# Kernel tuning notes

Measured on AMD Instinct MI355X. Metric: run time of the kernel, lower is better.

Reference implementation:

```python
import jax, jax.numpy as jnp
import numpy as np

K = 7  # SMorph filter size


def _smorph(x, w, alpha):
    # x: [B,1,H,W]; w: [K,K]; alpha: scalar
    # SMorph(x)(p) = sum_s (x(p+s)+w(s)) * exp(alpha*(x(p+s)+w(s))) / sum_s exp(...)
    patches = jax.lax.conv_general_dilated_patches(
        x, filter_shape=(K, K), window_strides=(1, 1), padding='SAME')  # [B,K*K,H,W]
    z = patches + w.reshape(1, K * K, 1, 1)
    wts = jax.nn.softmax(alpha * z, axis=1)
    out = jnp.sum(z * wts, axis=1, keepdims=True)  # [B,1,H,W]
    return out


def _pool2(x):
    # 2x2 average pool, stride 2; x: [...,H,W]
    B, C, H, W = x.shape
    return x.reshape(B, C, H // 2, 2, W // 2, 2).mean(axis=(3, 5))


def setup_inputs() -> dict:
    key = jax.random.key(0)
    ks = jax.random.split(key, 9)
    B = 512
    return {
        'x': jax.random.normal(ks[0], (B, 1, 28, 28), dtype=jnp.float32),
        'sm_w': 0.5 * jax.random.normal(ks[1], (8, 2, K, K), dtype=jnp.float32),
        'sm_alpha': jax.random.uniform(ks[2], (8, 2), dtype=jnp.float32),
        'W1': jax.random.normal(ks[3], (120, 392), dtype=jnp.float32) / np.sqrt(392),
        'b1': jax.random.normal(ks[4], (120,), dtype=jnp.float32) * 0.01,
        'W2': jax.random.normal(ks[5], (84, 120), dtype=jnp.float32) / np.sqrt(120),
        'b2': jax.random.normal(ks[6], (84,), dtype=jnp.float32) * 0.01,
        'W3': jax.random.normal(ks[7], (10, 84), dtype=jnp.float32) / np.sqrt(84),
        'b3': jax.random.normal(ks[8], (10,), dtype=jnp.float32) * 0.01,
    }


def reference(x, sm_w, sm_alpha, W1, b1, W2, b2, W3, b3):
    B = x.shape[0]

    def branch(w2, a2):
        y = _smorph(x, w2[0], a2[0])
        y = _smorph(y, w2[1], a2[1])
        y = _pool2(_pool2(y))  # [B,1,7,7]
        return y

    ys = jax.vmap(branch)(sm_w, sm_alpha)  # [8,B,1,7,7]
    feat = jnp.transpose(ys, (1, 0, 2, 3, 4)).reshape(B, -1)  # [B,392] = concat(x1..x8)
    h = jax.nn.sigmoid(feat @ W1.T + b1)
    h = jax.nn.sigmoid(h @ W2.T + b2)
    out = jax.nn.sigmoid(h @ W3.T + b3)
    return out
```

## Files before the change

### kernel.cpp

```cpp
#include <hip/hip_runtime.h>

#define HW 28
#define NPIX 784
#define NB 512
#define PADW2 34
#define PADH 34
#define IMG_U (PADH * PADW2)

__device__ __forceinline__ void conv2col(const unsigned* sbuf,
                                         unsigned wpack,
                                         int R0, int c, float o0[7], float o1[7])
{
    const uint2* rq0 = (const uint2*)(sbuf + R0 * PADW2 + 2 * c);
    uint2 p0 = rq0[0], p1 = rq0[1], p2 = rq0[2], p3 = rq0[3];

    unsigned Wq[49];
#pragma unroll
    for (int i = 0; i < 49; ++i)
        Wq[i] = __builtin_amdgcn_readlane(wpack, i);

    float num0[7], num1[7], den0[7], den1[7];
#pragma unroll
    for (int r = 0; r < 7; ++r) {
        num0[r] = 0.f; num1[r] = 0.f; den0[r] = 0.f; den1[r] = 0.f;
    }

#pragma unroll
    for (int rr = 0; rr < 13; ++rr) {
        uint2 n0, n1, n2, n3;
        if (rr < 12) {
            const uint2* rq = (const uint2*)(sbuf + (R0 + rr + 1) * PADW2 + 2 * c);
            n0 = rq[0]; n1 = rq[1]; n2 = rq[2]; n3 = rq[3];
            __builtin_amdgcn_sched_barrier(0);
        }
        unsigned tp[8] = {p0.x, p0.y, p1.x, p1.y, p2.x, p2.y, p3.x, p3.y};
#pragma unroll
        for (int r = 0; r < 7; ++r) {
            if (r > rr || rr - r > 6) continue;
            const int di = rr - r;
#pragma unroll
            for (int t = 0; t < 7; ++t) {
                unsigned wq = Wq[di * 7 + t];
                unsigned wd;
                asm("s_lshr_b32 %0, %1, 16" : "=s"(wd) : "s"(wq));
                asm("v_dot2_f32_f16 %0, %1, %2, %0"
                    : "+v"(num0[r]) : "v"(tp[t]),     "s"(wq));
                asm("v_dot2_f32_f16 %0, %1, %2, %0"
                    : "+v"(num1[r]) : "v"(tp[t + 1]), "s"(wq));
                asm("v_dot2_f32_f16 %0, %1, %2, %0"
                    : "+v"(den0[r]) : "v"(tp[t]),     "s"(wd));
                asm("v_dot2_f32_f16 %0, %1, %2, %0"
                    : "+v"(den1[r]) : "v"(tp[t + 1]), "s"(wd));
            }
        }
        if (rr < 12) { p0 = n0; p1 = n1; p2 = n2; p3 = n3; }
    }
#pragma unroll
    for (int r = 0; r < 7; ++r) {
        o0[r] = num0[r] * __builtin_amdgcn_rcpf(den0[r]);
        o1[r] = num1[r] * __builtin_amdgcn_rcpf(den1[r]);
    }
}

__device__ __forceinline__ float sigmoidf_(float s) {
    return __builtin_amdgcn_rcpf(1.f + __expf(-s));
}

__global__ __launch_bounds__(512, 2) void smorph_net_kernel(
    const float* __restrict__ x,
    const float* __restrict__ sw,
    const float* __restrict__ sa,
    const float* __restrict__ W1, const float* __restrict__ b1,
    const float* __restrict__ W2, const float* __restrict__ b2,
    const float* __restrict__ W3, const float* __restrict__ b3,
    float* __restrict__ out)
{
    __shared__ __align__(16) unsigned bufs[8][IMG_U];
    __shared__ __align__(16) float    mlp[392 + 120 + 128];

    const int b    = blockIdx.x;
    const int tid  = threadIdx.x;
    const int f    = tid >> 6;
    const int lane = tid & 63;

    unsigned* buf = bufs[f];
    const float* src = x + (size_t)b * NPIX;

    const float a1 = sa[f * 2 + 0];
    const float a2 = sa[f * 2 + 1];

    unsigned wp1 = 0, wp2 = 0;
    if (lane < 49) {
        union { _Float16 h[2]; unsigned u; } p;
        float w1v = sw[(f * 2 + 0) * 49 + lane];
        float e1  = __expf(a1 * w1v);
        p.h[0] = (_Float16)(w1v * e1);
        p.h[1] = (_Float16)e1;
        wp1 = p.u;
        float w2v = sw[(f * 2 + 1) * 49 + lane];
        float e2  = __expf(a2 * w2v);
        p.h[0] = (_Float16)(w2v * e2);
        p.h[1] = (_Float16)e2;
        wp2 = p.u;
    }

    for (int idx = lane; idx < IMG_U; idx += 64)
        buf[idx] = 0x00003C00u;

#pragma unroll
    for (int k = 0; k < 13; ++k) {
        int p = lane + 64 * k;
        if (p < NPIX) {
            float v = src[p];
            int pi = p / HW;
            int pj = p - pi * HW;
            float e = __expf(a1 * v);
            union { _Float16 h[2]; unsigned u; } pk;
            pk.h[0] = (_Float16)e;
            pk.h[1] = (_Float16)(v * e);
            buf[(pi + 3) * PADW2 + (pj + 3)] = pk.u;
        }
    }

    const bool act = (lane < 56);
    const int s  = lane / 14;
    const int c  = lane - s * 14;
    const int R0 = 7 * s;
    const int j2 = 2 * c;

    float o0[7], o1[7];
    if (act) conv2col(buf, wp1, R0, c, o0, o1);

    if (act) {
#pragma unroll
        for (int r = 0; r < 7; ++r) {
            union { _Float16 h[2]; unsigned u; } pk;
            float e0 = __expf(a2 * o0[r]);
            pk.h[0] = (_Float16)e0; pk.h[1] = (_Float16)(o0[r] * e0);
            buf[(R0 + r + 3) * PADW2 + (j2 + 3)] = pk.u;
            float e1 = __expf(a2 * o1[r]);
            pk.h[0] = (_Float16)e1; pk.h[1] = (_Float16)(o1[r] * e1);
            buf[(R0 + r + 3) * PADW2 + (j2 + 4)] = pk.u;
        }
    }

    if (act) conv2col(buf, wp2, R0, c, o0, o1);

    float* outp = (float*)buf;
    if (act) {
#pragma unroll
        for (int r = 0; r < 7; ++r) {
            outp[(R0 + r) * HW + j2]     = o0[r];
            outp[(R0 + r) * HW + j2 + 1] = o1[r];
        }
    }

    float* feat = mlp;
    float* h1   = mlp + 392;
    float* h2   = mlp + 512;

    if (lane < 49) {
        int pi = lane / 7;
        int pj = lane - pi * 7;
        float poolsum = 0.f;
#pragma unroll
        for (int di = 0; di < 4; ++di)
#pragma unroll
            for (int dj = 0; dj < 4; ++dj)
                poolsum += outp[(pi * 4 + di) * HW + (pj * 4 + dj)];
        feat[f * 49 + lane] = poolsum * 0.0625f;
    }
    __syncthreads();

    if (tid < 480) {
        int n = tid >> 2, h = tid & 3;
        const float4* wr = (const float4*)(W1 + n * 392);
        const float4* fv = (const float4*)feat;
        float c0 = 0.f, c1 = 0.f, c2 = 0.f, c3 = 0.f;
        for (int k = h; k < 98; k += 4) {
            float4 w = wr[k];
            float4 v = fv[k];
            c0 = fmaf(w.x, v.x, c0);
            c1 = fmaf(w.y, v.y, c1);
            c2 = fmaf(w.z, v.z, c2);
            c3 = fmaf(w.w, v.w, c3);
        }
        float acc = (c0 + c1) + (c2 + c3);
        acc += __shfl_xor(acc, 1);
        acc += __shfl_xor(acc, 2);
        if (h == 0) h1[n] = sigmoidf_(acc + b1[n]);
    }
    __syncthreads();

    if (tid < 336) {
        int n = tid >> 2, h = tid & 3;
        const float4* wr = (const float4*)(W2 + n * 120);
        const float4* hv = (const float4*)h1;
        float c0 = 0.f, c1 = 0.f, c2 = 0.f, c3 = 0.f;
        for (int k = h; k < 30; k += 4) {
            float4 w = wr[k];
            float4 v = hv[k];
            c0 = fmaf(w.x, v.x, c0);
            c1 = fmaf(w.y, v.y, c1);
            c2 = fmaf(w.z, v.z, c2);
            c3 = fmaf(w.w, v.w, c3);
        }
        float acc = (c0 + c1) + (c2 + c3);
        acc += __shfl_xor(acc, 1);
        acc += __shfl_xor(acc, 2);
        if (h == 0) h2[n] = sigmoidf_(acc + b2[n]);
    }
    __syncthreads();

    if (tid < 40) {
        int n = tid >> 2, q = tid & 3;
        const float4* wr = (const float4*)(W3 + n * 84);
        const float4* hv = (const float4*)h2;
        float c0 = 0.f, c1 = 0.f, c2 = 0.f, c3 = 0.f;
        for (int k = q; k < 21; k += 4) {
            float4 w = wr[k];
            float4 v = hv[k];
            c0 = fmaf(w.x, v.x, c0);
            c1 = fmaf(w.y, v.y, c1);
            c2 = fmaf(w.z, v.z, c2);
            c3 = fmaf(w.w, v.w, c3);
        }
        float acc = (c0 + c1) + (c2 + c3);
        acc += __shfl_xor(acc, 1);
        acc += __shfl_xor(acc, 2);
        if (q == 0) out[(size_t)b * 10 + n] = sigmoidf_(acc + b3[n]);
    }
}

extern "C" void kernel_launch(void* const* d_in, const int* in_sizes, int n_in,
                              void* d_out, int out_size, void* d_ws, size_t ws_size,
                              hipStream_t stream) {
    const float* x  = (const float*)d_in[0];
    const float* sw = (const float*)d_in[1];
    const float* sa = (const float*)d_in[2];
    const float* W1 = (const float*)d_in[3];
    const float* b1 = (const float*)d_in[4];
    const float* W2 = (const float*)d_in[5];
    const float* b2 = (const float*)d_in[6];
    const float* W3 = (const float*)d_in[7];
    const float* b3 = (const float*)d_in[8];
    float* out = (float*)d_out;

    smorph_net_kernel<<<NB, 512, 0, stream>>>(x, sw, sa, W1, b1, W2, b2, W3, b3, out);
}
```

Baseline: 101.1 us.

## Split each filter branch across two wavefronts, one output column each

```diff
diff --git a/kernel.cpp b/kernel.cpp
--- a/kernel.cpp
+++ b/kernel.cpp
@@ -7,9 +7,10 @@
 #define PADH 34
 #define IMG_U (PADH * PADW2)
 
-__device__ __forceinline__ void conv2col(const unsigned* sbuf,
+template<int P>
+__device__ __forceinline__ void conv1col(const unsigned* sbuf,
                                          unsigned wpack,
-                                         int R0, int c, float o0[7], float o1[7])
+                                         int R0, int c, float o[7])
 {
     const uint2* rq0 = (const uint2*)(sbuf + R0 * PADW2 + 2 * c);
     uint2 p0 = rq0[0], p1 = rq0[1], p2 = rq0[2], p3 = rq0[3];
@@ -19,11 +20,9 @@
     for (int i = 0; i < 49; ++i)
         Wq[i] = __builtin_amdgcn_readlane(wpack, i);
 
-    float num0[7], num1[7], den0[7], den1[7];
-#pragma unroll
-    for (int r = 0; r < 7; ++r) {
-        num0[r] = 0.f; num1[r] = 0.f; den0[r] = 0.f; den1[r] = 0.f;
-    }
+    float num[7], den[7];
+#pragma unroll
+    for (int r = 0; r < 7; ++r) { num[r] = 0.f; den[r] = 0.f; }
 
 #pragma unroll
     for (int rr = 0; rr < 13; ++rr) {
@@ -44,29 +43,23 @@
                 unsigned wd;
                 asm("s_lshr_b32 %0, %1, 16" : "=s"(wd) : "s"(wq));
                 asm("v_dot2_f32_f16 %0, %1, %2, %0"
-                    : "+v"(num0[r]) : "v"(tp[t]),     "s"(wq));
+                    : "+v"(num[r]) : "v"(tp[t + P]), "s"(wq));
                 asm("v_dot2_f32_f16 %0, %1, %2, %0"
-                    : "+v"(num1[r]) : "v"(tp[t + 1]), "s"(wq));
-                asm("v_dot2_f32_f16 %0, %1, %2, %0"
-                    : "+v"(den0[r]) : "v"(tp[t]),     "s"(wd));
-                asm("v_dot2_f32_f16 %0, %1, %2, %0"
-                    : "+v"(den1[r]) : "v"(tp[t + 1]), "s"(wd));
+                    : "+v"(den[r]) : "v"(tp[t + P]), "s"(wd));
             }
         }
         if (rr < 12) { p0 = n0; p1 = n1; p2 = n2; p3 = n3; }
     }
 #pragma unroll
-    for (int r = 0; r < 7; ++r) {
-        o0[r] = num0[r] * __builtin_amdgcn_rcpf(den0[r]);
-        o1[r] = num1[r] * __builtin_amdgcn_rcpf(den1[r]);
-    }
+    for (int r = 0; r < 7; ++r)
+        o[r] = num[r] * __builtin_amdgcn_rcpf(den[r]);
 }
 
 __device__ __forceinline__ float sigmoidf_(float s) {
     return __builtin_amdgcn_rcpf(1.f + __expf(-s));
 }
 
-__global__ __launch_bounds__(512, 2) void smorph_net_kernel(
+__global__ __launch_bounds__(1024, 2) void smorph_net_kernel(
     const float* __restrict__ x,
     const float* __restrict__ sw,
     const float* __restrict__ sa,
@@ -80,8 +73,10 @@
 
     const int b    = blockIdx.x;
     const int tid  = threadIdx.x;
-    const int f    = tid >> 6;
+    const int f    = tid >> 7;
+    const int t128 = tid & 127;
     const int lane = tid & 63;
+    const int P    = (t128 >> 6);
 
     unsigned* buf = bufs[f];
     const float* src = x + (size_t)b * NPIX;
@@ -104,12 +99,20 @@
         wp2 = p.u;
     }
 
-    for (int idx = lane; idx < IMG_U; idx += 64)
-        buf[idx] = 0x00003C00u;
-
-#pragma unroll
-    for (int k = 0; k < 13; ++k) {
-        int p = lane + 64 * k;
+    {
+        uint4* b4 = (uint4*)buf;
+        const uint4 fv = make_uint4(0x00003C00u, 0x00003C00u, 0x00003C00u, 0x00003C00u);
+#pragma unroll
+        for (int k = 0; k < 3; ++k) {
+            int i = t128 + 128 * k;
+            if (i < IMG_U / 4) b4[i] = fv;
+        }
+    }
+    __syncthreads();
+
+#pragma unroll
+    for (int k = 0; k < 7; ++k) {
+        int p = t128 + 128 * k;
         if (p < NPIX) {
             float v = src[p];
             int pi = p / HW;
@@ -121,45 +124,51 @@
             buf[(pi + 3) * PADW2 + (pj + 3)] = pk.u;
         }
     }
+    __syncthreads();
 
     const bool act = (lane < 56);
     const int s  = lane / 14;
     const int c  = lane - s * 14;
     const int R0 = 7 * s;
-    const int j2 = 2 * c;
-
-    float o0[7], o1[7];
-    if (act) conv2col(buf, wp1, R0, c, o0, o1);
+    const int j  = 2 * c + P;
+
+    float o[7];
+    if (act) {
+        if (P == 0) conv1col<0>(buf, wp1, R0, c, o);
+        else        conv1col<1>(buf, wp1, R0, c, o);
+    }
+    __syncthreads();
 
     if (act) {
 #pragma unroll
         for (int r = 0; r < 7; ++r) {
             union { _Float16 h[2]; unsigned u; } pk;
-            float e0 = __expf(a2 * o0[r]);
-            pk.h[0] = (_Float16)e0; pk.h[1] = (_Float16)(o0[r] * e0);
-            buf[(R0 + r + 3) * PADW2 + (j2 + 3)] = pk.u;
-            float e1 = __expf(a2 * o1[r]);
-            pk.h[0] = (_Float16)e1; pk.h[1] = (_Float16)(o1[r] * e1);
-            buf[(R0 + r + 3) * PADW2 + (j2 + 4)] = pk.u;
-        }
-    }
-
-    if (act) conv2col(buf, wp2, R0, c, o0, o1);
+            float e0 = __expf(a2 * o[r]);
+            pk.h[0] = (_Float16)e0; pk.h[1] = (_Float16)(o[r] * e0);
+            buf[(R0 + r + 3) * PADW2 + (j + 3)] = pk.u;
+        }
+    }
+    __syncthreads();
+
+    if (act) {
+        if (P == 0) conv1col<0>(buf, wp2, R0, c, o);
+        else        conv1col<1>(buf, wp2, R0, c, o);
+    }
+    __syncthreads();
 
     float* outp = (float*)buf;
     if (act) {
 #pragma unroll
-        for (int r = 0; r < 7; ++r) {
-            outp[(R0 + r) * HW + j2]     = o0[r];
-            outp[(R0 + r) * HW + j2 + 1] = o1[r];
-        }
-    }
+        for (int r = 0; r < 7; ++r)
+            outp[(R0 + r) * HW + j] = o[r];
+    }
+    __syncthreads();
 
     float* feat = mlp;
     float* h1   = mlp + 392;
     float* h2   = mlp + 512;
 
-    if (lane < 49) {
+    if (P == 0 && lane < 49) {
         int pi = lane / 7;
         int pj = lane - pi * 7;
         float poolsum = 0.f;
@@ -172,12 +181,12 @@
     }
     __syncthreads();
 
-    if (tid < 480) {
-        int n = tid >> 2, h = tid & 3;
+    if (tid < 960) {
+        int n = tid >> 3, h = tid & 7;
         const float4* wr = (const float4*)(W1 + n * 392);
         const float4* fv = (const float4*)feat;
         float c0 = 0.f, c1 = 0.f, c2 = 0.f, c3 = 0.f;
-        for (int k = h; k < 98; k += 4) {
+        for (int k = h; k < 98; k += 8) {
             float4 w = wr[k];
             float4 v = fv[k];
             c0 = fmaf(w.x, v.x, c0);
@@ -188,6 +197,7 @@
         float acc = (c0 + c1) + (c2 + c3);
         acc += __shfl_xor(acc, 1);
         acc += __shfl_xor(acc, 2);
+        acc += __shfl_xor(acc, 4);
         if (h == 0) h1[n] = sigmoidf_(acc + b1[n]);
     }
     __syncthreads();
@@ -246,5 +256,5 @@
     const float* b3 = (const float*)d_in[8];
     float* out = (float*)d_out;
 
-    smorph_net_kernel<<<NB, 512, 0, stream>>>(x, sw, sa, W1, b1, W2, b2, W3, b3, out);
-}
+    smorph_net_kernel<<<NB, 1024, 0, stream>>>(x, sw, sa, W1, b1, W2, b2, W3, b3, out);
+}
```

New measurement: 106.9 us. +5.7%, slower.

## Stage SMorph filter weights in LDS and loop over filter rows

Applied to the files above, without the earlier changes.

```diff
diff --git a/kernel.cpp b/kernel.cpp
--- a/kernel.cpp
+++ b/kernel.cpp
@@ -8,52 +8,49 @@
 #define IMG_U (PADH * PADW2)
 
 __device__ __forceinline__ void conv2col(const unsigned* sbuf,
-                                         unsigned wpack,
+                                         const unsigned* wlds,
                                          int R0, int c, float o0[7], float o1[7])
 {
-    const uint2* rq0 = (const uint2*)(sbuf + R0 * PADW2 + 2 * c);
-    uint2 p0 = rq0[0], p1 = rq0[1], p2 = rq0[2], p3 = rq0[3];
-
-    unsigned Wq[49];
-#pragma unroll
-    for (int i = 0; i < 49; ++i)
-        Wq[i] = __builtin_amdgcn_readlane(wpack, i);
-
     float num0[7], num1[7], den0[7], den1[7];
 #pragma unroll
     for (int r = 0; r < 7; ++r) {
         num0[r] = 0.f; num1[r] = 0.f; den0[r] = 0.f; den1[r] = 0.f;
     }
 
-#pragma unroll
-    for (int rr = 0; rr < 13; ++rr) {
-        uint2 n0, n1, n2, n3;
-        if (rr < 12) {
-            const uint2* rq = (const uint2*)(sbuf + (R0 + rr + 1) * PADW2 + 2 * c);
-            n0 = rq[0]; n1 = rq[1]; n2 = rq[2]; n3 = rq[3];
-            __builtin_amdgcn_sched_barrier(0);
-        }
-        unsigned tp[8] = {p0.x, p0.y, p1.x, p1.y, p2.x, p2.y, p3.x, p3.y};
+#pragma unroll 1
+    for (int di = 0; di < 7; ++di) {
+        const uint4* wp = (const uint4*)(wlds + di * 8);
+        uint4 wa = wp[0], wb = wp[1];
+        unsigned wq[7] = {wa.x, wa.y, wa.z, wa.w, wb.x, wb.y, wb.z};
+        unsigned wd[7];
+#pragma unroll
+        for (int t = 0; t < 7; ++t) wd[t] = wq[t] >> 16;
+
+        const uint2* rp = (const uint2*)(sbuf + (R0 + di) * PADW2 + 2 * c);
+        uint2 a0 = rp[0], a1 = rp[1], a2 = rp[2], a3 = rp[3];
+
 #pragma unroll
         for (int r = 0; r < 7; ++r) {
-            if (r > rr || rr - r > 6) continue;
-            const int di = rr - r;
+            uint2 b0, b1, b2, b3;
+            if (r < 6) {
+                const uint2* rn = (const uint2*)(sbuf + (R0 + di + r + 1) * PADW2 + 2 * c);
+                b0 = rn[0]; b1 = rn[1]; b2 = rn[2]; b3 = rn[3];
+                __builtin_amdgcn_sched_barrier(0);
+            }
+            unsigned tp[8] = {a0.x, a0.y, a1.x, a1.y, a2.x, a2.y, a3.x, a3.y};
 #pragma unroll
             for (int t = 0; t < 7; ++t) {
-                unsigned wq = Wq[di * 7 + t];
-                unsigned wd;
-                asm("s_lshr_b32 %0, %1, 16" : "=s"(wd) : "s"(wq));
-                asm("v_dot2_f32_f16 %0, %1, %2, %0"
-                    : "+v"(num0[r]) : "v"(tp[t]),     "s"(wq));
-                asm("v_dot2_f32_f16 %0, %1, %2, %0"
-                    : "+v"(num1[r]) : "v"(tp[t + 1]), "s"(wq));
-                asm("v_dot2_f32_f16 %0, %1, %2, %0"
-                    : "+v"(den0[r]) : "v"(tp[t]),     "s"(wd));
-                asm("v_dot2_f32_f16 %0, %1, %2, %0"
-                    : "+v"(den1[r]) : "v"(tp[t + 1]), "s"(wd));
+                asm("v_dot2_f32_f16 %0, %1, %2, %0"
+                    : "+v"(num0[r]) : "v"(tp[t]),     "v"(wq[t]));
+                asm("v_dot2_f32_f16 %0, %1, %2, %0"
+                    : "+v"(num1[r]) : "v"(tp[t + 1]), "v"(wq[t]));
+                asm("v_dot2_f32_f16 %0, %1, %2, %0"
+                    : "+v"(den0[r]) : "v"(tp[t]),     "v"(wd[t]));
+                asm("v_dot2_f32_f16 %0, %1, %2, %0"
+                    : "+v"(den1[r]) : "v"(tp[t + 1]), "v"(wd[t]));
             }
-        }
-        if (rr < 12) { p0 = n0; p1 = n1; p2 = n2; p3 = n3; }
+            if (r < 6) { a0 = b0; a1 = b1; a2 = b2; a3 = b3; }
+        }
     }
 #pragma unroll
     for (int r = 0; r < 7; ++r) {
@@ -76,6 +73,7 @@
     float* __restrict__ out)
 {
     __shared__ __align__(16) unsigned bufs[8][IMG_U];
+    __shared__ __align__(16) unsigned wtab[8][2][7][8];
     __shared__ __align__(16) float    mlp[392 + 120 + 128];
 
     const int b    = blockIdx.x;
@@ -89,19 +87,22 @@
     const float a1 = sa[f * 2 + 0];
     const float a2 = sa[f * 2 + 1];
 
-    unsigned wp1 = 0, wp2 = 0;
     if (lane < 49) {
+        int di = lane / 7, t = lane - di * 7;
         union { _Float16 h[2]; unsigned u; } p;
         float w1v = sw[(f * 2 + 0) * 49 + lane];
         float e1  = __expf(a1 * w1v);
         p.h[0] = (_Float16)(w1v * e1);
         p.h[1] = (_Float16)e1;
-        wp1 = p.u;
+        wtab[f][0][di][t] = p.u;
         float w2v = sw[(f * 2 + 1) * 49 + lane];
         float e2  = __expf(a2 * w2v);
         p.h[0] = (_Float16)(w2v * e2);
         p.h[1] = (_Float16)e2;
-        wp2 = p.u;
+        wtab[f][1][di][t] = p.u;
+    } else if (lane < 56) {
+        wtab[f][0][lane - 49][7] = 0u;
+        wtab[f][1][lane - 49][7] = 0u;
     }
 
     for (int idx = lane; idx < IMG_U; idx += 64)
@@ -129,7 +130,7 @@
     const int j2 = 2 * c;
 
     float o0[7], o1[7];
-    if (act) conv2col(buf, wp1, R0, c, o0, o1);
+    if (act) conv2col(buf, &wtab[f][0][0][0], R0, c, o0, o1);
 
     if (act) {
 #pragma unroll
@@ -144,7 +145,7 @@
         }
     }
 
-    if (act) conv2col(buf, wp2, R0, c, o0, o1);
+    if (act) conv2col(buf, &wtab[f][1][0][0], R0, c, o0, o1);
 
     float* outp = (float*)buf;
     if (act) {
```

New measurement: 101.7 us. No clear change (+0.6%).

## Recast SMorph 7x7 convolutions as MFMA f16 matrix products with banded weight tables

Applied to the files above, without the earlier changes.

```diff
diff --git a/kernel.cpp b/kernel.cpp
--- a/kernel.cpp
+++ b/kernel.cpp
@@ -3,63 +3,67 @@
 #define HW 28
 #define NPIX 784
 #define NB 512
-#define PADW2 34
-#define PADH 34
-#define IMG_U (PADH * PADW2)
-
-__device__ __forceinline__ void conv2col(const unsigned* sbuf,
-                                         unsigned wpack,
-                                         int R0, int c, float o0[7], float o1[7])
+#define PR 34
+#define PC 52
+#define PLANE (PR * PC)
+
+typedef _Float16 half8 __attribute__((ext_vector_type(8)));
+typedef float    f32x4 __attribute__((ext_vector_type(4)));
+
+union H8 { unsigned short s[8]; uint2 u2[2]; half8 h; };
+
+__device__ __forceinline__ void mconv(const _Float16 (*ev)[PC],
+                                      const _Float16 (*pv)[PC],
+                                      const unsigned short (*tbl)[7][48],
+                                      int q, int n15, f32x4 o[2][2])
 {
-    const uint2* rq0 = (const uint2*)(sbuf + R0 * PADW2 + 2 * c);
-    uint2 p0 = rq0[0], p1 = rq0[1], p2 = rq0[2], p3 = rq0[3];
-
-    unsigned Wq[49];
-#pragma unroll
-    for (int i = 0; i < 49; ++i)
-        Wq[i] = __builtin_amdgcn_readlane(wpack, i);
-
-    float num0[7], num1[7], den0[7], den1[7];
-#pragma unroll
-    for (int r = 0; r < 7; ++r) {
-        num0[r] = 0.f; num1[r] = 0.f; den0[r] = 0.f; den1[r] = 0.f;
-    }
-
-#pragma unroll
-    for (int rr = 0; rr < 13; ++rr) {
-        uint2 n0, n1, n2, n3;
-        if (rr < 12) {
-            const uint2* rq = (const uint2*)(sbuf + (R0 + rr + 1) * PADW2 + 2 * c);
-            n0 = rq[0]; n1 = rq[1]; n2 = rq[2]; n3 = rq[3];
-            __builtin_amdgcn_sched_barrier(0);
-        }
-        unsigned tp[8] = {p0.x, p0.y, p1.x, p1.y, p2.x, p2.y, p3.x, p3.y};
-#pragma unroll
-        for (int r = 0; r < 7; ++r) {
-            if (r > rr || rr - r > 6) continue;
-            const int di = rr - r;
-#pragma unroll
-            for (int t = 0; t < 7; ++t) {
-                unsigned wq = Wq[di * 7 + t];
-                unsigned wd;
-                asm("s_lshr_b32 %0, %1, 16" : "=s"(wd) : "s"(wq));
-                asm("v_dot2_f32_f16 %0, %1, %2, %0"
-                    : "+v"(num0[r]) : "v"(tp[t]),     "s"(wq));
-                asm("v_dot2_f32_f16 %0, %1, %2, %0"
-                    : "+v"(num1[r]) : "v"(tp[t + 1]), "s"(wq));
-                asm("v_dot2_f32_f16 %0, %1, %2, %0"
-                    : "+v"(den0[r]) : "v"(tp[t]),     "s"(wd));
-                asm("v_dot2_f32_f16 %0, %1, %2, %0"
-                    : "+v"(den1[r]) : "v"(tp[t + 1]), "s"(wd));
+    f32x4 num[2][2], den[2][2];
+#pragma unroll
+    for (int a = 0; a < 2; ++a)
+#pragma unroll
+        for (int c = 0; c < 2; ++c) {
+            num[a][c] = (f32x4){0.f, 0.f, 0.f, 0.f};
+            den[a][c] = (f32x4){0.f, 0.f, 0.f, 0.f};
+        }
+
+    const int bp = 16 + 4 * q - n15;
+
+#pragma unroll
+    for (int di = 0; di < 7; ++di) {
+        H8 bq, be;
+        const unsigned short* tq = &tbl[0][di][0];
+        const unsigned short* te = &tbl[1][di][0];
+#pragma unroll
+        for (int j = 0; j < 4; ++j) {
+            bq.s[j]     = tq[bp + j];
+            bq.s[4 + j] = tq[bp + 16 + j];
+            be.s[j]     = te[bp + j];
+            be.s[4 + j] = te[bp + 16 + j];
+        }
+#pragma unroll
+        for (int rt = 0; rt < 2; ++rt) {
+            const int row = rt * 12 + di + n15;
+#pragma unroll
+            for (int ct = 0; ct < 2; ++ct) {
+                const int col = ct * 16 + 4 * q;
+                H8 ea, pa;
+                ea.u2[0] = *(const uint2*)&ev[row][col];
+                ea.u2[1] = *(const uint2*)&ev[row][col + 16];
+                pa.u2[0] = *(const uint2*)&pv[row][col];
+                pa.u2[1] = *(const uint2*)&pv[row][col + 16];
+                num[rt][ct] = __builtin_amdgcn_mfma_f32_16x16x32_f16(ea.h, bq.h, num[rt][ct], 0, 0, 0);
+                num[rt][ct] = __builtin_amdgcn_mfma_f32_16x16x32_f16(pa.h, be.h, num[rt][ct], 0, 0, 0);
+                den[rt][ct] = __builtin_amdgcn_mfma_f32_16x16x32_f16(ea.h, be.h, den[rt][ct], 0, 0, 0);
             }
         }
-        if (rr < 12) { p0 = n0; p1 = n1; p2 = n2; p3 = n3; }
-    }
-#pragma unroll
-    for (int r = 0; r < 7; ++r) {
-        o0[r] = num0[r] * __builtin_amdgcn_rcpf(den0[r]);
-        o1[r] = num1[r] * __builtin_amdgcn_rcpf(den1[r]);
-    }
+    }
+#pragma unroll
+    for (int a = 0; a < 2; ++a)
+#pragma unroll
+        for (int c = 0; c < 2; ++c)
+#pragma unroll
+            for (int v = 0; v < 4; ++v)
+                o[a][c][v] = num[a][c][v] * __builtin_amdgcn_rcpf(den[a][c][v]);
 }
 
 __device__ __forceinline__ float sigmoidf_(float s) {
@@ -75,15 +79,19 @@
     const float* __restrict__ W3, const float* __restrict__ b3,
     float* __restrict__ out)
 {
-    __shared__ __align__(16) unsigned bufs[8][IMG_U];
-    __shared__ __align__(16) float    mlp[392 + 120 + 128];
+    __shared__ __align__(16) _Float16       planes[8][2][PR][PC];
+    __shared__ __align__(16) unsigned short wtbl[8][2][7][48];
+    __shared__ __align__(16) float          mlp[392 + 120 + 128];
 
     const int b    = blockIdx.x;
     const int tid  = threadIdx.x;
     const int f    = tid >> 6;
     const int lane = tid & 63;
-
-    unsigned* buf = bufs[f];
+    const int n15  = lane & 15;
+    const int q    = lane >> 4;
+
+    _Float16 (*ev)[PC] = planes[f][0];
+    _Float16 (*pv)[PC] = planes[f][1];
     const float* src = x + (size_t)b * NPIX;
 
     const float a1 = sa[f * 2 + 0];
@@ -104,8 +112,24 @@
         wp2 = p.u;
     }
 
-    for (int idx = lane; idx < IMG_U; idx += 64)
-        buf[idx] = 0x00003C00u;
+    {
+        unsigned* tz = (unsigned*)&wtbl[f][0][0][0];
+        for (int i = lane; i < 336; i += 64) tz[i] = 0;
+    }
+    if (lane < 49) {
+        int di = lane / 7, t = lane - di * 7;
+        wtbl[f][0][di][16 + t] = (unsigned short)(wp1 & 0xFFFF);
+        wtbl[f][1][di][16 + t] = (unsigned short)(wp1 >> 16);
+    }
+
+    {
+        unsigned* evu = (unsigned*)&planes[f][0][0][0];
+        unsigned* pvu = (unsigned*)&planes[f][1][0][0];
+        for (int i = lane; i < PLANE / 2; i += 64) {
+            evu[i] = 0x3C003C00u;
+            pvu[i] = 0u;
+        }
+    }
 
 #pragma unroll
     for (int k = 0; k < 13; ++k) {
@@ -115,61 +139,57 @@
             int pi = p / HW;
             int pj = p - pi * HW;
             float e = __expf(a1 * v);
-            union { _Float16 h[2]; unsigned u; } pk;
-            pk.h[0] = (_Float16)e;
-            pk.h[1] = (_Float16)(v * e);
-            buf[(pi + 3) * PADW2 + (pj + 3)] = pk.u;
-        }
-    }
-
-    const bool act = (lane < 56);
-    const int s  = lane / 14;
-    const int c  = lane - s * 14;
-    const int R0 = 7 * s;
-    const int j2 = 2 * c;
-
-    float o0[7], o1[7];
-    if (act) conv2col(buf, wp1, R0, c, o0, o1);
-
-    if (act) {
-#pragma unroll
-        for (int r = 0; r < 7; ++r) {
-            union { _Float16 h[2]; unsigned u; } pk;
-            float e0 = __expf(a2 * o0[r]);
-            pk.h[0] = (_Float16)e0; pk.h[1] = (_Float16)(o0[r] * e0);
-            buf[(R0 + r + 3) * PADW2 + (j2 + 3)] = pk.u;
-            float e1 = __expf(a2 * o1[r]);
-            pk.h[0] = (_Float16)e1; pk.h[1] = (_Float16)(o1[r] * e1);
-            buf[(R0 + r + 3) * PADW2 + (j2 + 4)] = pk.u;
-        }
-    }
-
-    if (act) conv2col(buf, wp2, R0, c, o0, o1);
-
-    float* outp = (float*)buf;
-    if (act) {
-#pragma unroll
-        for (int r = 0; r < 7; ++r) {
-            outp[(R0 + r) * HW + j2]     = o0[r];
-            outp[(R0 + r) * HW + j2 + 1] = o1[r];
-        }
-    }
+            ev[pi + 3][pj + 3] = (_Float16)e;
+            pv[pi + 3][pj + 3] = (_Float16)(v * e);
+        }
+    }
+
+    f32x4 o1_[2][2];
+    mconv(ev, pv, wtbl[f], q, n15, o1_);
+
+#pragma unroll
+    for (int rt = 0; rt < 2; ++rt)
+#pragma unroll
+        for (int ct = 0; ct < 2; ++ct) {
+            if (ct == 1 && n15 >= 12) continue;
+#pragma unroll
+            for (int v = 0; v < 4; ++v) {
+                int row = rt * 12 + 4 * q + v;
+                int col = ct * 16 + n15;
+                float ov = o1_[rt][ct][v];
+                float e  = __expf(a2 * ov);
+                ev[row + 3][col + 3] = (_Float16)e;
+                pv[row + 3][col + 3] = (_Float16)(ov * e);
+            }
+        }
+
+    if (lane < 49) {
+        int di = lane / 7, t = lane - di * 7;
+        wtbl[f][0][di][16 + t] = (unsigned short)(wp2 & 0xFFFF);
+        wtbl[f][1][di][16 + t] = (unsigned short)(wp2 >> 16);
+    }
+
+    f32x4 o2_[2][2];
+    mconv(ev, pv, wtbl[f], q, n15, o2_);
 
     float* feat = mlp;
     float* h1   = mlp + 392;
     float* h2   = mlp + 512;
 
-    if (lane < 49) {
-        int pi = lane / 7;
-        int pj = lane - pi * 7;
-        float poolsum = 0.f;
-#pragma unroll
-        for (int di = 0; di < 4; ++di)
-#pragma unroll
-            for (int dj = 0; dj < 4; ++dj)
-                poolsum += outp[(pi * 4 + di) * HW + (pj * 4 + dj)];
-        feat[f * 49 + lane] = poolsum * 0.0625f;
-    }
+#pragma unroll
+    for (int rt = 0; rt < 2; ++rt)
+#pragma unroll
+        for (int ct = 0; ct < 2; ++ct) {
+            float s = o2_[rt][ct][0] + o2_[rt][ct][1] + o2_[rt][ct][2] + o2_[rt][ct][3];
+            s += __shfl_xor(s, 1);
+            s += __shfl_xor(s, 2);
+            int pr = rt ? (3 + q) : q;
+            int pc = (ct ? 4 : 0) + (n15 >> 2);
+            bool ok = ((n15 & 3) == 0)
+                   && !(rt == 1 && q == 0)
+                   && !(ct == 1 && n15 >= 12);
+            if (ok) feat[f * 49 + pr * 7 + pc] = s * 0.0625f;
+        }
     __syncthreads();
 
     if (tid < 480) {
@@ -177,6 +197,7 @@
         const float4* wr = (const float4*)(W1 + n * 392);
         const float4* fv = (const float4*)feat;
         float c0 = 0.f, c1 = 0.f, c2 = 0.f, c3 = 0.f;
+#pragma unroll 2
         for (int k = h; k < 98; k += 4) {
             float4 w = wr[k];
             float4 v = fv[k];
@@ -213,11 +234,11 @@
     __syncthreads();
 
     if (tid < 40) {
-        int n = tid >> 2, q = tid & 3;
+        int n = tid >> 2, qh = tid & 3;
         const float4* wr = (const float4*)(W3 + n * 84);
         const float4* hv = (const float4*)h2;
         float c0 = 0.f, c1 = 0.f, c2 = 0.f, c3 = 0.f;
-        for (int k = q; k < 21; k += 4) {
+        for (int k = qh; k < 21; k += 4) {
             float4 w = wr[k];
             float4 v = hv[k];
             c0 = fmaf(w.x, v.x, c0);
@@ -228,7 +249,7 @@
         float acc = (c0 + c1) + (c2 + c3);
         acc += __shfl_xor(acc, 1);
         acc += __shfl_xor(acc, 2);
-        if (q == 0) out[(size_t)b * 10 + n] = sigmoidf_(acc + b3[n]);
+        if (qh == 0) out[(size_t)b * 10 + n] = sigmoidf_(acc + b3[n]);
     }
 }
 
```

New measurement: 106.4 us. +5.2%, slower.
